# Performance work log

Measured on AMD Instinct MI355X. Metric: run time of the kernel, lower is better.

Reference implementation:

```python
import jax, jax.numpy as jnp
import numpy as np

N = 100000      # nodes
E = 1600000     # edges (avg degree 16)
IN = 128        # in_feats
H = 4           # num_heads
F = 32          # out_feats per head
NEG_SLOPE = 0.2


def setup_inputs() -> dict:
    key = jax.random.key(0)
    k0, k1, k2, k3, k4, k5 = jax.random.split(key, 6)
    feat = jax.random.normal(k0, (N, IN), dtype=jnp.float32)
    # Glorot-ish scaled params
    W = jax.random.normal(k1, (IN, H * F), dtype=jnp.float32) * (1.0 / np.sqrt(IN))
    attn_l = jax.random.normal(k2, (H, F), dtype=jnp.float32) * 0.1
    attn_r = jax.random.normal(k3, (H, F), dtype=jnp.float32) * 0.1
    bias = jnp.zeros((H * F,), dtype=jnp.float32)
    src = jax.random.randint(k4, (E,), 0, N, dtype=jnp.int32)
    dst = jax.random.randint(k5, (E,), 0, N, dtype=jnp.int32)
    return {"feat": feat, "W": W, "attn_l": attn_l, "attn_r": attn_r,
            "bias": bias, "src": src, "dst": dst}


def reference(feat, W, attn_l, attn_r, bias, src, dst):
    # GeMM: projected features, [N, H, F]
    feat_src = (feat @ W).reshape(N, H, F)
    # per-node attention halves, [N, H]
    el = (feat_src * attn_l).sum(-1)
    er = (feat_src * attn_r).sum(-1)
    # per-edge score e_ij = LeakyReLU(el[src] + er[dst]), [E, H]
    e = el[src] + er[dst]
    e = jnp.where(e > 0, e, NEG_SLOPE * e)
    # edge softmax over destination-node segments (numerically stable)
    m = jax.ops.segment_max(e, dst, num_segments=N)          # [N, H]
    ex = jnp.exp(e - m[dst])                                  # [E, H]
    denom = jax.ops.segment_sum(ex, dst, num_segments=N)     # [N, H]
    alpha = ex / jnp.maximum(denom[dst], 1e-9)                # [E, H]
    # weighted SpMM aggregation: sum_j alpha_ij * Wh_j, [N, H, F]
    msg = feat_src[src] * alpha[:, :, None]                   # [E, H, F]
    rst = jax.ops.segment_sum(msg, dst, num_segments=N)      # [N, H, F]
    rst = rst + bias.reshape(1, H, F)
    return rst
```

## Files before the change

kernel.cpp:

```cpp
#include <hip/hip_runtime.h>
#include <hip/hip_fp16.h>

#define IN_F 128
#define HF   128
#define NH   4
#define NF   32

#define NPB       256
#define NPB_SHIFT 8
#define BIN_CHUNK 4096
#define HIST_BLOCKS 256
#define WFRAG_BLOCKS 8

typedef __attribute__((ext_vector_type(8))) short short8v;
typedef __attribute__((ext_vector_type(4))) float f32x4;

__device__ __forceinline__ unsigned short f32_to_bf16_rtn(float f) {
    unsigned int u = __float_as_uint(f);
    u += 0x7fffu + ((u >> 16) & 1u);
    return (unsigned short)(u >> 16);
}

#define FMA_MIX_LO(acc, pair, w) \
    asm("v_fma_mix_f32 %0, %1, %2, %0 op_sel:[0,0,0] op_sel_hi:[1,0,0]" \
        : "+v"(acc) : "v"(pair), "v"(w))
#define FMA_MIX_HI(acc, pair, w) \
    asm("v_fma_mix_f32 %0, %1, %2, %0 op_sel:[1,0,0] op_sel_hi:[1,0,0]" \
        : "+v"(acc) : "v"(pair), "v"(w))

__global__ void __launch_bounds__(256)
gat_wfrag_hist(const float* __restrict__ W, short8v* __restrict__ wfrag,
               const int* __restrict__ dst, int* __restrict__ bcount,
               int E, int nbuck, int chunk) {
    const int t = threadIdx.x;
    if ((int)blockIdx.x < WFRAG_BLOCKS) {
        const int entry = blockIdx.x * 256 + t;
        const int lane = entry & 63;
        const int kb   = (entry >> 6) & 3;
        const int nt   = entry >> 8;
        const int k0   = kb * 32 + (lane >> 4) * 8;
        const int col  = nt * 16 + (lane & 15);
        short8v s;
        #pragma unroll
        for (int j = 0; j < 8; ++j)
            s[j] = (short)f32_to_bf16_rtn(W[(k0 + j) * HF + col]);
        wfrag[entry] = s;
        return;
    }
    __shared__ int h[512];
    for (int i = t; i < 512; i += 256) h[i] = 0;
    __syncthreads();
    const int hb = blockIdx.x - WFRAG_BLOCKS;
    const int e0 = hb * chunk;
    const int e1 = min(e0 + chunk, E);
    for (int e = e0 + t; e < e1; e += 256)
        atomicAdd(&h[dst[e] >> NPB_SHIFT], 1);
    __syncthreads();
    for (int b = t; b < nbuck; b += 256)
        if (h[b]) atomicAdd(&bcount[b], h[b]);
}

__global__ void __launch_bounds__(512)
gat_bucket_scan(const int* __restrict__ bcount, int* __restrict__ bbase,
                int* __restrict__ gcursor, int* __restrict__ offsets,
                int N, int E, int nbuck) {
    __shared__ int buf[512];
    const int t = threadIdx.x;
    int v = (t < nbuck) ? bcount[t] : 0;
    buf[t] = v;
    __syncthreads();
    for (int off = 1; off < 512; off <<= 1) {
        int x = (t >= off) ? buf[t - off] : 0;
        __syncthreads();
        buf[t] += x;
        __syncthreads();
    }
    if (t < nbuck) {
        int base = buf[t] - v;
        bbase[t]   = base;
        gcursor[t] = base;
    }
    if (t == 0) {
        bbase[nbuck] = E;
        offsets[N]   = E;
    }
}

__global__ void __launch_bounds__(256)
gat_bin_gemm(const int* __restrict__ src, const int* __restrict__ dst,
             int* __restrict__ gcursor, unsigned int* __restrict__ gpairs, int E,
             int nBin,
             const float* __restrict__ feat, const short8v* __restrict__ wfrag,
             const float* __restrict__ attn_l, const float* __restrict__ attn_r,
             unsigned short* __restrict__ feat_src_h,
             float* __restrict__ el, float* __restrict__ er, int N) {
    __shared__ __align__(16) char smem[49152];
    const int t = threadIdx.x;

    if ((int)blockIdx.x < nBin) {
        unsigned int*   stage  = (unsigned int*)smem;
        unsigned short* buckof = (unsigned short*)(smem + 16384);
        int* hist  = (int*)(smem + 24576);
        int* sc    = (int*)(smem + 26624);
        int* basew = (int*)(smem + 28672);
        int* cur   = (int*)(smem + 30720);
        for (int i = t; i < 512; i += 256) hist[i] = 0;
        __syncthreads();
        const int e0  = blockIdx.x * BIN_CHUNK;
        const int cnt = min(BIN_CHUNK, E - e0);
        for (int i = t; i < cnt; i += 256)
            atomicAdd(&hist[dst[e0 + i] >> NPB_SHIFT], 1);
        __syncthreads();
        sc[t]       = hist[t];
        sc[t + 256] = hist[t + 256];
        __syncthreads();
        for (int off = 1; off < 512; off <<= 1) {
            int x0 = (t >= off) ? sc[t - off] : 0;
            int x1 = sc[t + 256 - off];
            __syncthreads();
            sc[t]       += x0;
            sc[t + 256] += x1;
            __syncthreads();
        }
        for (int b = t; b < 512; b += 256) {
            int c  = hist[b];
            int ex = sc[b] - c;
            cur[b] = ex;
            basew[b] = c ? atomicAdd(&gcursor[b], c) : 0;
        }
        __syncthreads();
        for (int i = t; i < cnt; i += 256) {
            unsigned s = (unsigned)src[e0 + i];
            unsigned d = (unsigned)dst[e0 + i];
            int b = (int)(d >> NPB_SHIFT);
            int p = atomicAdd(&cur[b], 1);
            stage[p]  = (s << 8) | (d & (NPB - 1));
            buckof[p] = (unsigned short)b;
        }
        __syncthreads();
        for (int j = t; j < cnt; j += 256) {
            int b  = (int)buckof[j];
            int ex = sc[b] - hist[b];
            gpairs[basew[b] + (j - ex)] = stage[j];
        }
        return;
    }

    unsigned short* a_lds = (unsigned short*)smem;
    unsigned short* w_lds = (unsigned short*)(smem + 16384);
    const int lane = t & 63;
    const int wave = t >> 6;
    const int row0b = (blockIdx.x - nBin) * 64;

    {
        const uint4* wsrc = (const uint4*)wfrag;
        uint4* wdst = (uint4*)w_lds;
        #pragma unroll
        for (int i = 0; i < 8; ++i)
            wdst[i * 256 + t] = wsrc[i * 256 + t];
    }
    #pragma unroll
    for (int i = 0; i < 8; ++i) {
        int idx = i * 256 + t;
        int row = idx >> 5;
        int c4  = idx & 31;
        int srow = min(row0b + row, N - 1);
        float4 f = *(const float4*)(feat + (size_t)srow * IN_F + c4 * 4);
        unsigned int lo = ((unsigned int)f32_to_bf16_rtn(f.y) << 16) | f32_to_bf16_rtn(f.x);
        unsigned int hi = ((unsigned int)f32_to_bf16_rtn(f.w) << 16) | f32_to_bf16_rtn(f.z);
        int kb = c4 >> 3, g = (c4 >> 1) & 3, half = c4 & 1;
        int wv = row >> 4, m = row & 15;
        unsigned int* p = (unsigned int*)a_lds;
        int u = (wv * 4096 + kb * 1024 + g * 256 + m * 16 + half * 8) >> 2;
        p[u]     = lo;
        p[u + 1] = hi;
    }
    __syncthreads();

    const int m = lane & 15;
    const int g = lane >> 4;
    short8v aw[4];
    #pragma unroll
    for (int kb = 0; kb < 4; ++kb)
        aw[kb] = *(const short8v*)&a_lds[wave * 2048 + kb * 512 + g * 128 + m * 8];

    f32x4 acc[8];
    #pragma unroll
    for (int nt = 0; nt < 8; ++nt) acc[nt] = (f32x4){0.f, 0.f, 0.f, 0.f};

    #pragma unroll
    for (int nt = 0; nt < 8; ++nt) {
        #pragma unroll
        for (int kb = 0; kb < 4; ++kb) {
            short8v bw = *(const short8v*)&w_lds[((nt * 4 + kb) * 64 + lane) * 8];
            acc[nt] = __builtin_amdgcn_mfma_f32_16x16x32_bf16(aw[kb], bw, acc[nt], 0, 0, 0);
        }
    }

    float al[8], ar[8];
    #pragma unroll
    for (int nt = 0; nt < 8; ++nt) {
        al[nt] = attn_l[nt * 16 + m];
        ar[nt] = attn_r[nt * 16 + m];
    }

    #pragma unroll
    for (int r = 0; r < 4; ++r) {
        const int row = row0b + wave * 16 + 4 * g + r;
        const bool valid = (row < N);
        if (valid) {
            #pragma unroll
            for (int nt = 0; nt < 8; ++nt)
                feat_src_h[(size_t)row * HF + nt * 16 + m] =
                    __half_as_ushort(__float2half(acc[nt][r]));
        }
        float pl[NH], pr[NH];
        #pragma unroll
        for (int h = 0; h < NH; ++h) {
            pl[h] = acc[2 * h][r] * al[2 * h] + acc[2 * h + 1][r] * al[2 * h + 1];
            pr[h] = acc[2 * h][r] * ar[2 * h] + acc[2 * h + 1][r] * ar[2 * h + 1];
        }
        #pragma unroll
        for (int mask = 1; mask <= 8; mask <<= 1) {
            #pragma unroll
            for (int h = 0; h < NH; ++h) {
                pl[h] += __shfl_xor(pl[h], mask);
                pr[h] += __shfl_xor(pr[h], mask);
            }
        }
        if (valid && m == 0) {
            *(float4*)(el + (size_t)row * NH) = make_float4(pl[0], pl[1], pl[2], pl[3]);
            *(float4*)(er + (size_t)row * NH) = make_float4(pr[0], pr[1], pr[2], pr[3]);
        }
    }
}

__global__ void __launch_bounds__(256)
gat_fine(const unsigned int* __restrict__ gpairs, const int* __restrict__ bbase,
         int* __restrict__ offsets, int* __restrict__ slot, int N) {
    __shared__ int h[NPB];
    __shared__ int buf[NPB];
    __shared__ int cur[NPB];
    const int b     = blockIdx.x;
    const int node0 = b << NPB_SHIFT;
    const int t     = threadIdx.x;
    const int beg = bbase[b];
    const int end = bbase[b + 1];
    h[t] = 0;
    __syncthreads();
    for (int i = beg + t; i < end; i += 256)
        atomicAdd(&h[gpairs[i] & (NPB - 1)], 1);
    __syncthreads();
    int v = h[t];
    buf[t] = v;
    __syncthreads();
    for (int off = 1; off < 256; off <<= 1) {
        int x = (t >= off) ? buf[t - off] : 0;
        __syncthreads();
        buf[t] += x;
        __syncthreads();
    }
    int ex = buf[t] - v;
    if (node0 + t < N) offsets[node0 + t] = beg + ex;
    cur[t] = ex;
    __syncthreads();
    for (int i = beg + t; i < end; i += 256) {
        unsigned pr = gpairs[i];
        int p = atomicAdd(&cur[pr & (NPB - 1)], 1);
        slot[beg + p] = (int)(pr >> 8);
    }
}

__global__ void __launch_bounds__(256)
gat_aggregate(const unsigned short* __restrict__ feat_src_h,
              const float* __restrict__ el, const float* __restrict__ er,
              const int* __restrict__ offsets, const int* __restrict__ slot,
              const float* __restrict__ bias, float* __restrict__ out, int N) {
    __shared__ int   ss[4][64];
    __shared__ float exs[4][256];
    const int lane = threadIdx.x & 63;
    const int wave = threadIdx.x >> 6;
    const int node = blockIdx.x * 4 + wave;
    if (node >= N) return;
    const int start = offsets[node];
    const int end   = offsets[node + 1];
    const int k  = lane & 15;
    const int g  = lane >> 4;
    const int hm = k >> 2;

    const float4 er4 = *(const float4*)(er + (size_t)node * NH);
    float d0 = 0.f, d1 = 0.f, d2 = 0.f, d3 = 0.f;
    float ax0 = 0.f, ax1 = 0.f, ax2 = 0.f, ax3 = 0.f;
    float ax4 = 0.f, ax5 = 0.f, ax6 = 0.f, ax7 = 0.f;
    const unsigned short* fsp = feat_src_h + 8 * k;
    int*   ssw = ss[wave];
    float* exw = exs[wave];

    for (int c = start; c < end; c += 64) {
        int idx = c + lane;
        bool vld = idx < end;
        int s_l = vld ? slot[idx] : 0;
        float4 ev = make_float4(0.f, 0.f, 0.f, 0.f);
        if (vld) ev = *(const float4*)(el + (size_t)s_l * NH);
        float x0 = ev.x + er4.x; x0 = fmaxf(x0, 0.2f * x0);
        float x1 = ev.y + er4.y; x1 = fmaxf(x1, 0.2f * x1);
        float x2 = ev.z + er4.z; x2 = fmaxf(x2, 0.2f * x2);
        float x3 = ev.w + er4.w; x3 = fmaxf(x3, 0.2f * x3);
        float e0 = vld ? __expf(x0) : 0.f;
        float e1 = vld ? __expf(x1) : 0.f;
        float e2 = vld ? __expf(x2) : 0.f;
        float e3 = vld ? __expf(x3) : 0.f;
        d0 += e0; d1 += e1; d2 += e2; d3 += e3;
        ssw[lane] = s_l;
        *(float4*)&exw[lane * 4] = make_float4(e0, e1, e2, e3);
        asm volatile("" ::: "memory");
        const int n = min(64, end - c);
        int j = g;
        for (; j + 4 < n; j += 8) {
            int jB = j + 4;
            int sA = ssw[j];
            int sB = ssw[jB];
            float wA = exw[j * 4 + hm];
            float wB = exw[jB * 4 + hm];
            uint4 uA = *(const uint4*)(fsp + (size_t)sA * HF);
            uint4 uB = *(const uint4*)(fsp + (size_t)sB * HF);
            FMA_MIX_LO(ax0, uA.x, wA); FMA_MIX_LO(ax0, uB.x, wB);
            FMA_MIX_HI(ax1, uA.x, wA); FMA_MIX_HI(ax1, uB.x, wB);
            FMA_MIX_LO(ax2, uA.y, wA); FMA_MIX_LO(ax2, uB.y, wB);
            FMA_MIX_HI(ax3, uA.y, wA); FMA_MIX_HI(ax3, uB.y, wB);
            FMA_MIX_LO(ax4, uA.z, wA); FMA_MIX_LO(ax4, uB.z, wB);
            FMA_MIX_HI(ax5, uA.z, wA); FMA_MIX_HI(ax5, uB.z, wB);
            FMA_MIX_LO(ax6, uA.w, wA); FMA_MIX_LO(ax6, uB.w, wB);
            FMA_MIX_HI(ax7, uA.w, wA); FMA_MIX_HI(ax7, uB.w, wB);
        }
        if (j < n) {
            int sA = ssw[j];
            float wA = exw[j * 4 + hm];
            uint4 uA = *(const uint4*)(fsp + (size_t)sA * HF);
            FMA_MIX_LO(ax0, uA.x, wA);
            FMA_MIX_HI(ax1, uA.x, wA);
            FMA_MIX_LO(ax2, uA.y, wA);
            FMA_MIX_HI(ax3, uA.y, wA);
            FMA_MIX_LO(ax4, uA.z, wA);
            FMA_MIX_HI(ax5, uA.z, wA);
            FMA_MIX_LO(ax6, uA.w, wA);
            FMA_MIX_HI(ax7, uA.w, wA);
        }
        asm volatile("" ::: "memory");
    }

    #pragma unroll
    for (int msk = 16; msk <= 32; msk <<= 1) {
        ax0 += __shfl_xor(ax0, msk); ax1 += __shfl_xor(ax1, msk);
        ax2 += __shfl_xor(ax2, msk); ax3 += __shfl_xor(ax3, msk);
        ax4 += __shfl_xor(ax4, msk); ax5 += __shfl_xor(ax5, msk);
        ax6 += __shfl_xor(ax6, msk); ax7 += __shfl_xor(ax7, msk);
    }

    #pragma unroll
    for (int msk = 1; msk <= 32; msk <<= 1) {
        d0 += __shfl_xor(d0, msk);
        d1 += __shfl_xor(d1, msk);
        d2 += __shfl_xor(d2, msk);
        d3 += __shfl_xor(d3, msk);
    }
    float dh = (hm == 0) ? d0 : (hm == 1) ? d1 : (hm == 2) ? d2 : d3;
    const float inv = 1.0f / fmaxf(dh, 1e-9f);

    if (g == 0) {
        float4 b0 = *(const float4*)(bias + 8 * k);
        float4 b1 = *(const float4*)(bias + 8 * k + 4);
        float4 o0, o1;
        o0.x = ax0 * inv + b0.x; o0.y = ax1 * inv + b0.y;
        o0.z = ax2 * inv + b0.z; o0.w = ax3 * inv + b0.w;
        o1.x = ax4 * inv + b1.x; o1.y = ax5 * inv + b1.y;
        o1.z = ax6 * inv + b1.z; o1.w = ax7 * inv + b1.w;
        *(float4*)(out + (size_t)node * HF + 8 * k)     = o0;
        *(float4*)(out + (size_t)node * HF + 8 * k + 4) = o1;
    }
}

extern "C" void kernel_launch(void* const* d_in, const int* in_sizes, int n_in,
                              void* d_out, int out_size, void* d_ws, size_t ws_size,
                              hipStream_t stream) {
    const float* feat   = (const float*)d_in[0];
    const float* W      = (const float*)d_in[1];
    const float* attn_l = (const float*)d_in[2];
    const float* attn_r = (const float*)d_in[3];
    const float* bias   = (const float*)d_in[4];
    const int*   src    = (const int*)d_in[5];
    const int*   dst    = (const int*)d_in[6];
    float* out = (float*)d_out;

    const int N = in_sizes[0] / IN_F;
    const int E = in_sizes[5];
    const int nbuck = (N + NPB - 1) / NPB;

    char* ws = (char*)d_ws;
    size_t off = 0;
    auto alloc = [&](size_t bytes) -> void* {
        off = (off + 255) & ~(size_t)255;
        void* p = ws + off;
        off += bytes;
        return p;
    };
    unsigned short* feat_src_h = (unsigned short*)alloc((size_t)N * HF * sizeof(unsigned short));
    float* el      = (float*)alloc((size_t)N * NH * sizeof(float));
    float* er      = (float*)alloc((size_t)N * NH * sizeof(float));
    int*   bcount  = (int*)  alloc((size_t)(nbuck + 1) * sizeof(int));
    int*   bbase   = (int*)  alloc((size_t)(nbuck + 1) * sizeof(int));
    int*   gcursor = (int*)  alloc((size_t)nbuck * sizeof(int));
    int*   offsets = (int*)  alloc((size_t)(N + 1) * sizeof(int));
    unsigned int* gpairs = (unsigned int*)alloc((size_t)E * sizeof(unsigned int));
    int*   slot    = (int*)  alloc((size_t)E * sizeof(int));
    short8v* wfrag = (short8v*)alloc((size_t)2048 * sizeof(short8v));

    hipMemsetAsync(bcount, 0, (size_t)(nbuck + 1) * sizeof(int), stream);

    const int chunk1 = (E + HIST_BLOCKS - 1) / HIST_BLOCKS;
    gat_wfrag_hist<<<WFRAG_BLOCKS + HIST_BLOCKS, 256, 0, stream>>>(
        W, wfrag, dst, bcount, E, nbuck, chunk1);

    gat_bucket_scan<<<1, 512, 0, stream>>>(bcount, bbase, gcursor, offsets, N, E, nbuck);

    const int nBin = (E + BIN_CHUNK - 1) / BIN_CHUNK;
    const int gemmBlocks = (N + 63) / 64;
    gat_bin_gemm<<<nBin + gemmBlocks, 256, 0, stream>>>(
        src, dst, gcursor, gpairs, E, nBin,
        feat, wfrag, attn_l, attn_r, feat_src_h, el, er, N);

    gat_fine<<<nbuck, 256, 0, stream>>>(gpairs, bbase, offsets, slot, N);

    gat_aggregate<<<(N + 3) / 4, 256, 0, stream>>>(feat_src_h, el, er, offsets, slot, bias, out, N);
}
```

Measured before the change: 147.1 us.

## Split GEMM blocks across bin and fine kernels; accumulate softmax denominator in aggregation loop

The projection GEMM work is now split: three fifths of the row tiles stay in the binning kernel and the rest run as extra blocks in the fine-sort kernel. This balances the two launches so the GEMM fills idle compute while the bandwidth-bound sort phases run. In the aggregation, the softmax denominator is summed per lane from the same exp weights used for the FMAs, replacing four per-head accumulators and a full 64-lane reduction with one value reduced alongside the feature accumulators. The fine kernel now reserves 48KB of shared memory, which may lower its occupancy.

```diff
diff --git a/kernel.cpp b/kernel.cpp
--- a/kernel.cpp
+++ b/kernel.cpp
@@ -27,6 +27,100 @@
 #define FMA_MIX_HI(acc, pair, w) \
     asm("v_fma_mix_f32 %0, %1, %2, %0 op_sel:[1,0,0] op_sel_hi:[1,0,0]" \
         : "+v"(acc) : "v"(pair), "v"(w))
+
+__device__ __forceinline__ void gemm_body(
+    int row0b, char* smem,
+    const float* __restrict__ feat, const short8v* __restrict__ wfrag,
+    const float* __restrict__ attn_l, const float* __restrict__ attn_r,
+    unsigned short* __restrict__ feat_src_h,
+    float* __restrict__ el, float* __restrict__ er, int N, int t) {
+    unsigned short* a_lds = (unsigned short*)smem;
+    unsigned short* w_lds = (unsigned short*)(smem + 16384);
+    const int lane = t & 63;
+    const int wave = t >> 6;
+
+    {
+        const uint4* wsrc = (const uint4*)wfrag;
+        uint4* wdst = (uint4*)w_lds;
+        #pragma unroll
+        for (int i = 0; i < 8; ++i)
+            wdst[i * 256 + t] = wsrc[i * 256 + t];
+    }
+    #pragma unroll
+    for (int i = 0; i < 8; ++i) {
+        int idx = i * 256 + t;
+        int row = idx >> 5;
+        int c4  = idx & 31;
+        int srow = min(row0b + row, N - 1);
+        float4 f = *(const float4*)(feat + (size_t)srow * IN_F + c4 * 4);
+        unsigned int lo = ((unsigned int)f32_to_bf16_rtn(f.y) << 16) | f32_to_bf16_rtn(f.x);
+        unsigned int hi = ((unsigned int)f32_to_bf16_rtn(f.w) << 16) | f32_to_bf16_rtn(f.z);
+        int kb = c4 >> 3, g = (c4 >> 1) & 3, half = c4 & 1;
+        int wv = row >> 4, m = row & 15;
+        unsigned int* p = (unsigned int*)a_lds;
+        int u = (wv * 4096 + kb * 1024 + g * 256 + m * 16 + half * 8) >> 2;
+        p[u]     = lo;
+        p[u + 1] = hi;
+    }
+    __syncthreads();
+
+    const int m = lane & 15;
+    const int g = lane >> 4;
+    short8v aw[4];
+    #pragma unroll
+    for (int kb = 0; kb < 4; ++kb)
+        aw[kb] = *(const short8v*)&a_lds[wave * 2048 + kb * 512 + g * 128 + m * 8];
+
+    f32x4 acc[8];
+    #pragma unroll
+    for (int nt = 0; nt < 8; ++nt) acc[nt] = (f32x4){0.f, 0.f, 0.f, 0.f};
+
+    #pragma unroll
+    for (int nt = 0; nt < 8; ++nt) {
+        #pragma unroll
+        for (int kb = 0; kb < 4; ++kb) {
+            short8v bw = *(const short8v*)&w_lds[((nt * 4 + kb) * 64 + lane) * 8];
+            acc[nt] = __builtin_amdgcn_mfma_f32_16x16x32_bf16(aw[kb], bw, acc[nt], 0, 0, 0);
+        }
+    }
+
+    float al[8], ar[8];
+    #pragma unroll
+    for (int nt = 0; nt < 8; ++nt) {
+        al[nt] = attn_l[nt * 16 + m];
+        ar[nt] = attn_r[nt * 16 + m];
+    }
+
+    #pragma unroll
+    for (int r = 0; r < 4; ++r) {
+        const int row = row0b + wave * 16 + 4 * g + r;
+        const bool valid = (row < N);
+        if (valid) {
+            #pragma unroll
+            for (int nt = 0; nt < 8; ++nt)
+                feat_src_h[(size_t)row * HF + nt * 16 + m] =
+                    __half_as_ushort(__float2half(acc[nt][r]));
+        }
+        float pl[NH], pr[NH];
+        #pragma unroll
+        for (int h = 0; h < NH; ++h) {
+            pl[h] = acc[2 * h][r] * al[2 * h] + acc[2 * h + 1][r] * al[2 * h + 1];
+            pr[h] = acc[2 * h][r] * ar[2 * h] + acc[2 * h + 1][r] * ar[2 * h + 1];
+        }
+        #pragma unroll
+        for (int mask = 1; mask <= 8; mask <<= 1) {
+            #pragma unroll
+            for (int h = 0; h < NH; ++h) {
+                pl[h] += __shfl_xor(pl[h], mask);
+                pr[h] += __shfl_xor(pr[h], mask);
+            }
+        }
+        if (valid && m == 0) {
+            *(float4*)(el + (size_t)row * NH) = make_float4(pl[0], pl[1], pl[2], pl[3]);
+            *(float4*)(er + (size_t)row * NH) = make_float4(pr[0], pr[1], pr[2], pr[3]);
+        }
+    }
+}
 
 __global__ void __launch_bounds__(256)
 gat_wfrag_hist(const float* __restrict__ W, short8v* __restrict__ wfrag,
@@ -146,129 +240,56 @@
         return;
     }
 
-    unsigned short* a_lds = (unsigned short*)smem;
-    unsigned short* w_lds = (unsigned short*)(smem + 16384);
-    const int lane = t & 63;
-    const int wave = t >> 6;
-    const int row0b = (blockIdx.x - nBin) * 64;
-
-    {
-        const uint4* wsrc = (const uint4*)wfrag;
-        uint4* wdst = (uint4*)w_lds;
-        #pragma unroll
-        for (int i = 0; i < 8; ++i)
-            wdst[i * 256 + t] = wsrc[i * 256 + t];
-    }
-    #pragma unroll
-    for (int i = 0; i < 8; ++i) {
-        int idx = i * 256 + t;
-        int row = idx >> 5;
-        int c4  = idx & 31;
-        int srow = min(row0b + row, N - 1);
-        float4 f = *(const float4*)(feat + (size_t)srow * IN_F + c4 * 4);
-        unsigned int lo = ((unsigned int)f32_to_bf16_rtn(f.y) << 16) | f32_to_bf16_rtn(f.x);
-        unsigned int hi = ((unsigned int)f32_to_bf16_rtn(f.w) << 16) | f32_to_bf16_rtn(f.z);
-        int kb = c4 >> 3, g = (c4 >> 1) & 3, half = c4 & 1;
-        int wv = row >> 4, m = row & 15;
-        unsigned int* p = (unsigned int*)a_lds;
-        int u = (wv * 4096 + kb * 1024 + g * 256 + m * 16 + half * 8) >> 2;
-        p[u]     = lo;
-        p[u + 1] = hi;
-    }
-    __syncthreads();
-
-    const int m = lane & 15;
-    const int g = lane >> 4;
-    short8v aw[4];
-    #pragma unroll
-    for (int kb = 0; kb < 4; ++kb)
-        aw[kb] = *(const short8v*)&a_lds[wave * 2048 + kb * 512 + g * 128 + m * 8];
-
-    f32x4 acc[8];
-    #pragma unroll
-    for (int nt = 0; nt < 8; ++nt) acc[nt] = (f32x4){0.f, 0.f, 0.f, 0.f};
-
-    #pragma unroll
-    for (int nt = 0; nt < 8; ++nt) {
-        #pragma unroll
-        for (int kb = 0; kb < 4; ++kb) {
-            short8v bw = *(const short8v*)&w_lds[((nt * 4 + kb) * 64 + lane) * 8];
-            acc[nt] = __builtin_amdgcn_mfma_f32_16x16x32_bf16(aw[kb], bw, acc[nt], 0, 0, 0);
-        }
-    }
-
-    float al[8], ar[8];
-    #pragma unroll
-    for (int nt = 0; nt < 8; ++nt) {
-        al[nt] = attn_l[nt * 16 + m];
-        ar[nt] = attn_r[nt * 16 + m];
-    }
-
-    #pragma unroll
-    for (int r = 0; r < 4; ++r) {
-        const int row = row0b + wave * 16 + 4 * g + r;
-        const bool valid = (row < N);
-        if (valid) {
-            #pragma unroll
-            for (int nt = 0; nt < 8; ++nt)
-                feat_src_h[(size_t)row * HF + nt * 16 + m] =
-                    __half_as_ushort(__float2half(acc[nt][r]));
-        }
-        float pl[NH], pr[NH];
-        #pragma unroll
-        for (int h = 0; h < NH; ++h) {
-            pl[h] = acc[2 * h][r] * al[2 * h] + acc[2 * h + 1][r] * al[2 * h + 1];
-            pr[h] = acc[2 * h][r] * ar[2 * h] + acc[2 * h + 1][r] * ar[2 * h + 1];
-        }
-        #pragma unroll
-        for (int mask = 1; mask <= 8; mask <<= 1) {
-            #pragma unroll
-            for (int h = 0; h < NH; ++h) {
-                pl[h] += __shfl_xor(pl[h], mask);
-                pr[h] += __shfl_xor(pr[h], mask);
-            }
-        }
-        if (valid && m == 0) {
-            *(float4*)(el + (size_t)row * NH) = make_float4(pl[0], pl[1], pl[2], pl[3]);
-            *(float4*)(er + (size_t)row * NH) = make_float4(pr[0], pr[1], pr[2], pr[3]);
-        }
-    }
+    gemm_body((blockIdx.x - nBin) * 64, smem, feat, wfrag, attn_l, attn_r,
+              feat_src_h, el, er, N, t);
 }
 
 __global__ void __launch_bounds__(256)
-gat_fine(const unsigned int* __restrict__ gpairs, const int* __restrict__ bbase,
-         int* __restrict__ offsets, int* __restrict__ slot, int N) {
-    __shared__ int h[NPB];
-    __shared__ int buf[NPB];
-    __shared__ int cur[NPB];
-    const int b     = blockIdx.x;
-    const int node0 = b << NPB_SHIFT;
-    const int t     = threadIdx.x;
-    const int beg = bbase[b];
-    const int end = bbase[b + 1];
-    h[t] = 0;
-    __syncthreads();
-    for (int i = beg + t; i < end; i += 256)
-        atomicAdd(&h[gpairs[i] & (NPB - 1)], 1);
-    __syncthreads();
-    int v = h[t];
-    buf[t] = v;
-    __syncthreads();
-    for (int off = 1; off < 256; off <<= 1) {
-        int x = (t >= off) ? buf[t - off] : 0;
-        __syncthreads();
-        buf[t] += x;
-        __syncthreads();
-    }
-    int ex = buf[t] - v;
-    if (node0 + t < N) offsets[node0 + t] = beg + ex;
-    cur[t] = ex;
-    __syncthreads();
-    for (int i = beg + t; i < end; i += 256) {
-        unsigned pr = gpairs[i];
-        int p = atomicAdd(&cur[pr & (NPB - 1)], 1);
-        slot[beg + p] = (int)(pr >> 8);
-    }
+gat_fine_gemm(const unsigned int* __restrict__ gpairs, const int* __restrict__ bbase,
+              int* __restrict__ offsets, int* __restrict__ slot, int nFine, int gemmA,
+              const float* __restrict__ feat, const short8v* __restrict__ wfrag,
+              const float* __restrict__ attn_l, const float* __restrict__ attn_r,
+              unsigned short* __restrict__ feat_src_h,
+              float* __restrict__ el, float* __restrict__ er, int N) {
+    __shared__ __align__(16) char smem[49152];
+    const int t = threadIdx.x;
+
+    if ((int)blockIdx.x < nFine) {
+        int* h   = (int*)smem;
+        int* buf = (int*)(smem + 1024);
+        int* cur = (int*)(smem + 2048);
+        const int b     = blockIdx.x;
+        const int node0 = b << NPB_SHIFT;
+        const int beg = bbase[b];
+        const int end = bbase[b + 1];
+        h[t] = 0;
+        __syncthreads();
+        for (int i = beg + t; i < end; i += 256)
+            atomicAdd(&h[gpairs[i] & (NPB - 1)], 1);
+        __syncthreads();
+        int v = h[t];
+        buf[t] = v;
+        __syncthreads();
+        for (int off = 1; off < 256; off <<= 1) {
+            int x = (t >= off) ? buf[t - off] : 0;
+            __syncthreads();
+            buf[t] += x;
+            __syncthreads();
+        }
+        int ex = buf[t] - v;
+        if (node0 + t < N) offsets[node0 + t] = beg + ex;
+        cur[t] = ex;
+        __syncthreads();
+        for (int i = beg + t; i < end; i += 256) {
+            unsigned pr = gpairs[i];
+            int p = atomicAdd(&cur[pr & (NPB - 1)], 1);
+            slot[beg + p] = (int)(pr >> 8);
+        }
+        return;
+    }
+
+    gemm_body((gemmA + (int)blockIdx.x - nFine) * 64, smem, feat, wfrag,
+              attn_l, attn_r, feat_src_h, el, er, N, t);
 }
 
 __global__ void __launch_bounds__(256)
@@ -289,7 +310,7 @@
     const int hm = k >> 2;
 
     const float4 er4 = *(const float4*)(er + (size_t)node * NH);
-    float d0 = 0.f, d1 = 0.f, d2 = 0.f, d3 = 0.f;
+    float dacc = 0.f;
     float ax0 = 0.f, ax1 = 0.f, ax2 = 0.f, ax3 = 0.f;
     float ax4 = 0.f, ax5 = 0.f, ax6 = 0.f, ax7 = 0.f;
     const unsigned short* fsp = feat_src_h + 8 * k;
@@ -310,7 +331,6 @@
         float e1 = vld ? __expf(x1) : 0.f;
         float e2 = vld ? __expf(x2) : 0.f;
         float e3 = vld ? __expf(x3) : 0.f;
-        d0 += e0; d1 += e1; d2 += e2; d3 += e3;
         ssw[lane] = s_l;
         *(float4*)&exw[lane * 4] = make_float4(e0, e1, e2, e3);
         asm volatile("" ::: "memory");
@@ -324,6 +344,7 @@
             float wB = exw[jB * 4 + hm];
             uint4 uA = *(const uint4*)(fsp + (size_t)sA * HF);
             uint4 uB = *(const uint4*)(fsp + (size_t)sB * HF);
+            dacc += wA + wB;
             FMA_MIX_LO(ax0, uA.x, wA); FMA_MIX_LO(ax0, uB.x, wB);
             FMA_MIX_HI(ax1, uA.x, wA); FMA_MIX_HI(ax1, uB.x, wB);
             FMA_MIX_LO(ax2, uA.y, wA); FMA_MIX_LO(ax2, uB.y, wB);
@@ -337,6 +358,7 @@
             int sA = ssw[j];
             float wA = exw[j * 4 + hm];
             uint4 uA = *(const uint4*)(fsp + (size_t)sA * HF);
+            dacc += wA;
             FMA_MIX_LO(ax0, uA.x, wA);
             FMA_MIX_HI(ax1, uA.x, wA);
             FMA_MIX_LO(ax2, uA.y, wA);
@@ -355,17 +377,9 @@
         ax2 += __shfl_xor(ax2, msk); ax3 += __shfl_xor(ax3, msk);
         ax4 += __shfl_xor(ax4, msk); ax5 += __shfl_xor(ax5, msk);
         ax6 += __shfl_xor(ax6, msk); ax7 += __shfl_xor(ax7, msk);
-    }
-
-    #pragma unroll
-    for (int msk = 1; msk <= 32; msk <<= 1) {
-        d0 += __shfl_xor(d0, msk);
-        d1 += __shfl_xor(d1, msk);
-        d2 += __shfl_xor(d2, msk);
-        d3 += __shfl_xor(d3, msk);
-    }
-    float dh = (hm == 0) ? d0 : (hm == 1) ? d1 : (hm == 2) ? d2 : d3;
-    const float inv = 1.0f / fmaxf(dh, 1e-9f);
+        dacc += __shfl_xor(dacc, msk);
+    }
+    const float inv = 1.0f / fmaxf(dacc, 1e-9f);
 
     if (g == 0) {
         float4 b0 = *(const float4*)(bias + 8 * k);
@@ -425,11 +439,15 @@
 
     const int nBin = (E + BIN_CHUNK - 1) / BIN_CHUNK;
     const int gemmBlocks = (N + 63) / 64;
-    gat_bin_gemm<<<nBin + gemmBlocks, 256, 0, stream>>>(
+    const int gemmA = (gemmBlocks * 3) / 5;
+    const int gemmB = gemmBlocks - gemmA;
+    gat_bin_gemm<<<nBin + gemmA, 256, 0, stream>>>(
         src, dst, gcursor, gpairs, E, nBin,
         feat, wfrag, attn_l, attn_r, feat_src_h, el, er, N);
 
-    gat_fine<<<nbuck, 256, 0, stream>>>(gpairs, bbase, offsets, slot, N);
+    gat_fine_gemm<<<nbuck + gemmB, 256, 0, stream>>>(
+        gpairs, bbase, offsets, slot, nbuck, gemmA,
+        feat, wfrag, attn_l, attn_r, feat_src_h, el, er, N);
 
     gat_aggregate<<<(N + 3) / 4, 256, 0, stream>>>(feat_src_h, el, er, offsets, slot, bias, out, N);
 }
```

Result: faster. 141.6 us (-3.7%).
